# Optimization experiments

Hardware: AMD Instinct MI355X
Metric: run time of the kernel (lower is better)

## Reference

```python
import jax, jax.numpy as jnp
import numpy as np

NB_HEAD = 16
DIM_PER_HEAD = 64
EMB = 1024
B, SQ, SK = 4, 2048, 2048


def setup_inputs() -> dict:
    key = jax.random.key(0)
    ks = jax.random.split(key, 8)
    scale = 1.0 / np.sqrt(EMB)
    return {
        "hidden_state_query": jax.random.normal(ks[0], (B, SQ, EMB), jnp.float32),
        "hidden_state_key": jax.random.normal(ks[1], (B, SK, EMB), jnp.float32),
        "hidden_state_value": jax.random.normal(ks[2], (B, SK, EMB), jnp.float32),
        "attention_mask": jax.random.randint(ks[3], (B, SQ, SK), 0, 2).astype(bool),
        "Wq": jax.random.uniform(ks[4], (NB_HEAD * DIM_PER_HEAD, EMB), jnp.float32, -scale, scale),
        "Wk": jax.random.uniform(ks[5], (NB_HEAD * DIM_PER_HEAD, EMB), jnp.float32, -scale, scale),
        "Wv": jax.random.uniform(ks[6], (NB_HEAD * DIM_PER_HEAD, EMB), jnp.float32, -scale, scale),
        "Wo": jax.random.uniform(ks[7], (EMB, NB_HEAD * DIM_PER_HEAD), jnp.float32, -scale, scale),
    }


def reference(hidden_state_query, hidden_state_key, hidden_state_value,
              attention_mask, Wq, Wk, Wv, Wo):
    bs, sq, _ = hidden_state_query.shape
    sk = hidden_state_key.shape[1]
    # projections (nn.Linear without bias: x @ W.T)
    q = (hidden_state_query @ Wq.T).reshape(bs, sq, NB_HEAD, DIM_PER_HEAD).transpose(0, 2, 1, 3)
    k = (hidden_state_key @ Wk.T).reshape(bs, sk, NB_HEAD, DIM_PER_HEAD).transpose(0, 2, 1, 3)
    v = (hidden_state_value @ Wv.T).reshape(bs, sk, NB_HEAD, DIM_PER_HEAD).transpose(0, 2, 1, 3)
    scores = jnp.einsum('bhqd,bhkd->bhqk', q, k) / jnp.sqrt(jnp.asarray(DIM_PER_HEAD, q.dtype))
    attn = jax.nn.softmax(scores, axis=-1)
    # POST-softmax zero masking (True -> 0), broadcast over heads; no renormalization
    attn = jnp.where(attention_mask[:, None, :, :], jnp.asarray(0.0, attn.dtype), attn)
    ctx = jnp.einsum('bhqk,bhkd->bhqd', attn, v)  # [B,H,Sq,Dh]
    ctx = ctx.transpose(0, 2, 1, 3).reshape(bs, sq, NB_HEAD * DIM_PER_HEAD)
    return ctx @ Wo.T + hidden_state_query
```

## Files before the change

### kernel.cpp

```cpp
#include <hip/hip_runtime.h>
#include <hip/hip_bf16.h>
#include <stdint.h>

typedef __bf16 bf16_t;
typedef bf16_t bf16x2 __attribute__((ext_vector_type(2)));
typedef bf16_t bf16x8 __attribute__((ext_vector_type(8)));
typedef float  f32x4  __attribute__((ext_vector_type(4)));
typedef float  f32x16 __attribute__((ext_vector_type(16)));
typedef unsigned uint2v __attribute__((ext_vector_type(2)));

#define NB_HEAD 16
#define DH      64
#define EMB     1024
#define BATCH   4
#define SEQ     2048
#define NTOK    (BATCH*SEQ)

#define QSCALE 0.1803368801111204f

__device__ __forceinline__ void gload_lds16(const void* g, void* l) {
  __builtin_amdgcn_global_load_lds(
      (const __attribute__((address_space(1))) void*)g,
      (__attribute__((address_space(3))) void*)l, 16, 0, 0);
}

__device__ __forceinline__ uint32_t pkbf(float a, float b) {
  bf16x2 v = { (bf16_t)a, (bf16_t)b };
  return __builtin_bit_cast(uint32_t, v);
}

__device__ __forceinline__ void cvt8_body(const float* __restrict__ in,
                                          bf16_t* __restrict__ out, int i) {
  const float4* p = reinterpret_cast<const float4*>(in) + (size_t)i * 2;
  float4 a = p[0], b = p[1];
  uint4 r;
  r.x = pkbf(a.x, a.y); r.y = pkbf(a.z, a.w);
  r.z = pkbf(b.x, b.y); r.w = pkbf(b.z, b.w);
  reinterpret_cast<uint4*>(out)[i] = r;
}

__device__ __forceinline__ void mkand_body(const uint8_t* __restrict__ m,
                                           uint16_t* __restrict__ out, int i) {
  uint2 v = reinterpret_cast<const uint2*>(m)[i];
  uint4 r;
  uint32_t lo = v.x, hi = v.y;
  uint16_t e[8];
#pragma unroll
  for (int j = 0; j < 4; j++) e[j]     = (uint16_t)(((lo >> (8 * j)) & 0xFF) - 1);
#pragma unroll
  for (int j = 0; j < 4; j++) e[4 + j] = (uint16_t)(((hi >> (8 * j)) & 0xFF) - 1);
  r.x = (uint32_t)e[0] | ((uint32_t)e[1] << 16);
  r.y = (uint32_t)e[2] | ((uint32_t)e[3] << 16);
  r.z = (uint32_t)e[4] | ((uint32_t)e[5] << 16);
  r.w = (uint32_t)e[6] | ((uint32_t)e[7] << 16);
  reinterpret_cast<uint4*>(out)[i] = r;
}

__global__ void __launch_bounds__(256)
prep(const float* __restrict__ Wq, const float* __restrict__ Wk,
     const float* __restrict__ Wv, const float* __restrict__ Wo,
     bf16_t* Wq_b, bf16_t* Wk_b, bf16_t* Wv_b, bf16_t* Wo_b,
     const uint8_t* __restrict__ mask, uint16_t* __restrict__ mand) {
  const int bid = blockIdx.x;
  if (bid < 2048) {
    const int seg = bid >> 9;
    const float* src = seg == 0 ? Wq : seg == 1 ? Wk : seg == 2 ? Wv : Wo;
    bf16_t*      dst = seg == 0 ? Wq_b : seg == 1 ? Wk_b : seg == 2 ? Wv_b : Wo_b;
    cvt8_body(src, dst, (bid & 511) * 256 + (int)threadIdx.x);
  } else {
    mkand_body(mask, mand, (bid - 2048) * 256 + (int)threadIdx.x);
  }
}

#define BM 128
#define BN 128
#define BKT 32

__global__ void __launch_bounds__(256, 2)
gemm_qkv(const float* __restrict__ hq, const float* __restrict__ hk,
         const float* __restrict__ hv,
         const bf16_t* __restrict__ Wq_b, const bf16_t* __restrict__ Wk_b,
         const bf16_t* __restrict__ Wv_b,
         bf16_t* __restrict__ Qb, bf16_t* __restrict__ Kf,
         bf16_t* __restrict__ Vf) {
  __shared__ bf16_t As[2][BM * BKT];
  __shared__ bf16_t Bs[2][BN * BKT];
  const int K = EMB;
  const int z = blockIdx.z;
  const float*  A  = z == 0 ? hq : z == 1 ? hk : hv;
  const bf16_t* Bw = z == 0 ? Wq_b : z == 1 ? Wk_b : Wv_b;

  const int t    = threadIdx.x;
  const int lane = t & 63, w = t >> 6;
  const int wr = w >> 1, wc = w & 1;
  const int l15 = lane & 15, l4 = lane >> 4;

  const int lin = blockIdx.x + 8 * blockIdx.y;
  const int nl  = (lin & 7) * 64 + (lin >> 3);
  const int rowBase = (nl >> 3) * BM, colBase = (nl & 7) * BN;

  f32x4 acc[4][4];
#pragma unroll
  for (int i = 0; i < 4; i++)
#pragma unroll
    for (int j = 0; j < 4; j++) acc[i][j] = f32x4{0.f, 0.f, 0.f, 0.f};

  const int t16 = t * 16;
  const int ar = t >> 1, ac = (t & 1) * 16;
  const float* arow = A + (size_t)(rowBase + ar) * K + ac;
  char* const asdst0 = (char*)As[0] + ar * 64 + ac * 2;
  char* const asdst1 = (char*)As[1] + ar * 64 + ac * 2;

  {
    float4 a0 = *reinterpret_cast<const float4*>(arow);
    float4 a1 = *reinterpret_cast<const float4*>(arow + 4);
    float4 a2 = *reinterpret_cast<const float4*>(arow + 8);
    float4 a3 = *reinterpret_cast<const float4*>(arow + 12);
#pragma unroll
    for (int i = 0; i < 2; ++i) {
      int off = i * 4096 + t16;
      int row = off >> 6, colb = off & 63;
      gload_lds16((const char*)Bw + (((size_t)(colBase + row)) * K) * 2 + colb, (char*)Bs[0] + off);
    }
    uint4 w0, w1;
    w0.x = pkbf(a0.x, a0.y); w0.y = pkbf(a0.z, a0.w);
    w0.z = pkbf(a1.x, a1.y); w0.w = pkbf(a1.z, a1.w);
    w1.x = pkbf(a2.x, a2.y); w1.y = pkbf(a2.z, a2.w);
    w1.z = pkbf(a3.x, a3.y); w1.w = pkbf(a3.z, a3.w);
    *reinterpret_cast<uint4*>(asdst0) = w0;
    *reinterpret_cast<uint4*>(asdst0 + 16) = w1;
  }
  __syncthreads();

  int cur = 0;
  for (int k0 = 0; k0 < K; k0 += BKT) {
    float4 na0, na1, na2, na3;
    const bool more = (k0 + BKT < K);
    if (more) {
      const float* ap = arow + k0 + BKT;
      na0 = *reinterpret_cast<const float4*>(ap);
      na1 = *reinterpret_cast<const float4*>(ap + 4);
      na2 = *reinterpret_cast<const float4*>(ap + 8);
      na3 = *reinterpret_cast<const float4*>(ap + 12);
      const int nb = cur ^ 1;
#pragma unroll
      for (int i = 0; i < 2; ++i) {
        int off = i * 4096 + t16;
        int row = off >> 6, colb = off & 63;
        gload_lds16((const char*)Bw + (((size_t)(colBase + row)) * K + k0 + BKT) * 2 + colb, (char*)Bs[nb] + off);
      }
    }
    {
      bf16x8 af[4], bfb[4];
#pragma unroll
      for (int mi = 0; mi < 4; mi++)
        af[mi] = *reinterpret_cast<const bf16x8*>(
            &As[cur][(wr * 64 + mi * 16 + l15) * BKT + l4 * 8]);
#pragma unroll
      for (int ni = 0; ni < 4; ni++)
        bfb[ni] = *reinterpret_cast<const bf16x8*>(
            &Bs[cur][(wc * 64 + ni * 16 + l15) * BKT + l4 * 8]);
      __builtin_amdgcn_s_setprio(1);
#pragma unroll
      for (int mi = 0; mi < 4; mi++)
#pragma unroll
        for (int ni = 0; ni < 4; ni++)
          acc[mi][ni] = __builtin_amdgcn_mfma_f32_16x16x32_bf16(
              af[mi], bfb[ni], acc[mi][ni], 0, 0, 0);
      __builtin_amdgcn_s_setprio(0);
    }
    if (more) {
      uint4 w0, w1;
      w0.x = pkbf(na0.x, na0.y); w0.y = pkbf(na0.z, na0.w);
      w0.z = pkbf(na1.x, na1.y); w0.w = pkbf(na1.z, na1.w);
      w1.x = pkbf(na2.x, na2.y); w1.y = pkbf(na2.z, na2.w);
      w1.z = pkbf(na3.x, na3.y); w1.w = pkbf(na3.z, na3.w);
      char* d = (cur ? asdst0 : asdst1);
      *reinterpret_cast<uint4*>(d) = w0;
      *reinterpret_cast<uint4*>(d + 16) = w1;
    }
    __syncthreads();
    cur ^= 1;
  }

#pragma unroll
  for (int mi = 0; mi < 4; mi++) {
#pragma unroll
    for (int ni = 0; ni < 4; ni++) {
      const int m0 = rowBase + wr * 64 + mi * 16 + l4 * 4;
      const int n  = colBase + wc * 64 + ni * 16 + l15;
      if (z == 0) {
#pragma unroll
        for (int r = 0; r < 4; r++)
          Qb[(size_t)(m0 + r) * EMB + n] = (bf16_t)(acc[mi][ni][r] * QSCALE);
      } else if (z == 1) {
#pragma unroll
        for (int r = 0; r < 4; r++) {
          int m = m0 + r;
          const int bq = m >> 11, s = m & 2047, hh = n >> 6, d = n & 63;
          size_t local = (size_t)(s >> 6) * 4096 + ((s >> 5) & 1) * 2048 +
                         (d >> 4) * 512 + ((d >> 3) & 1) * 256 + (s & 31) * 8 + (d & 7);
          Kf[(size_t)(bq * 16 + hh) * 131072 + local] = (bf16_t)acc[mi][ni][r];
        }
      } else {
        const int bq = m0 >> 11, s0 = m0 & 2047, hh = n >> 6, d = n & 63;
        size_t local = (size_t)(s0 >> 6) * 4096 + ((s0 >> 4) & 3) * 1024 +
                       (d >> 5) * 512 + ((s0 >> 3) & 1) * 256 + (d & 31) * 8 + (s0 & 7);
        uint2 st;
        st.x = pkbf(acc[mi][ni][0], acc[mi][ni][1]);
        st.y = pkbf(acc[mi][ni][2], acc[mi][ni][3]);
        *reinterpret_cast<uint2*>(Vf + (size_t)(bq * 16 + hh) * 131072 + local) = st;
      }
    }
  }
}

__global__ void __launch_bounds__(256, 4)
gemm_out(const bf16_t* __restrict__ A, const bf16_t* __restrict__ Bw,
         float* __restrict__ Cf, const float* __restrict__ resid) {
  __shared__ bf16_t As[2][BM * BKT];
  __shared__ bf16_t Bs[2][BN * BKT];
  const int K = EMB, N = EMB;
  const int t    = threadIdx.x;
  const int lane = t & 63, w = t >> 6;
  const int wr = w >> 1, wc = w & 1;
  const int l15 = lane & 15, l4 = lane >> 4;

  const int lin = blockIdx.x + 8 * blockIdx.y;
  const int nl  = (lin & 7) * 64 + (lin >> 3);
  const int rowBase = (nl >> 3) * BM, colBase = (nl & 7) * BN;

  f32x4 acc[4][4];
#pragma unroll
  for (int i = 0; i < 4; i++)
#pragma unroll
    for (int j = 0; j < 4; j++) acc[i][j] = f32x4{0.f, 0.f, 0.f, 0.f};

  const int t16 = t * 16;

#pragma unroll
  for (int i = 0; i < 2; ++i) {
    int off = i * 4096 + t16;
    int row = off >> 6, colb = off & 63;
    gload_lds16((const char*)A  + (((size_t)(rowBase + row)) * K) * 2 + colb, (char*)As[0] + off);
    gload_lds16((const char*)Bw + (((size_t)(colBase + row)) * K) * 2 + colb, (char*)Bs[0] + off);
  }
  __syncthreads();

  int cur = 0;
  for (int k0 = 0; k0 < K; k0 += BKT) {
    if (k0 + BKT < K) {
      const int nb = cur ^ 1;
#pragma unroll
      for (int i = 0; i < 2; ++i) {
        int off = i * 4096 + t16;
        int row = off >> 6, colb = off & 63;
        gload_lds16((const char*)A  + (((size_t)(rowBase + row)) * K + k0 + BKT) * 2 + colb, (char*)As[nb] + off);
        gload_lds16((const char*)Bw + (((size_t)(colBase + row)) * K + k0 + BKT) * 2 + colb, (char*)Bs[nb] + off);
      }
    }
    {
      bf16x8 af[4], bfb[4];
#pragma unroll
      for (int mi = 0; mi < 4; mi++)
        af[mi] = *reinterpret_cast<const bf16x8*>(
            &As[cur][(wr * 64 + mi * 16 + l15) * BKT + l4 * 8]);
#pragma unroll
      for (int ni = 0; ni < 4; ni++)
        bfb[ni] = *reinterpret_cast<const bf16x8*>(
            &Bs[cur][(wc * 64 + ni * 16 + l15) * BKT + l4 * 8]);
      __builtin_amdgcn_s_setprio(1);
#pragma unroll
      for (int mi = 0; mi < 4; mi++)
#pragma unroll
        for (int ni = 0; ni < 4; ni++)
          acc[mi][ni] = __builtin_amdgcn_mfma_f32_16x16x32_bf16(
              af[mi], bfb[ni], acc[mi][ni], 0, 0, 0);
      __builtin_amdgcn_s_setprio(0);
    }
    __syncthreads();
    cur ^= 1;
  }

#pragma unroll
  for (int mi = 0; mi < 4; mi++) {
#pragma unroll
    for (int ni = 0; ni < 4; ni++) {
      const int m0 = rowBase + wr * 64 + mi * 16 + l4 * 4;
      const int n  = colBase + wc * 64 + ni * 16 + l15;
#pragma unroll
      for (int r = 0; r < 4; r++) {
        int m = m0 + r;
        Cf[(size_t)m * N + n] = acc[mi][ni][r] + resid[(size_t)m * N + n];
      }
    }
  }
}

__global__ void __launch_bounds__(512, 2)
attn32(const bf16_t* __restrict__ Qb, const bf16_t* __restrict__ Kh,
       const bf16_t* __restrict__ Vt, const uint16_t* __restrict__ Mand,
       bf16_t* __restrict__ ctx) {
  __shared__ __align__(16) bf16_t Ks[2][64 * 64];
  __shared__ __align__(16) bf16_t Vs[2][64 * 64];

  const int t = threadIdx.x, lane = t & 63, wid = t >> 6;
  const int q = lane & 31, hi = lane >> 5;
  const int l16 = lane * 16;

  const int lin = blockIdx.x + 8 * (blockIdx.y + 16 * blockIdx.z);
  const int nl  = (lin & 7) * 64 + (lin >> 3);
  const int bx = nl & 7, h = (nl >> 3) & 15, b = nl >> 7;

  const int q0 = bx * 256 + wid * 32;
  const int qrow = b * SEQ + q0 + q;

  const char* kg = (const char*)(Kh + ((size_t)(b * NB_HEAD + h)) * SEQ * DH);
  const char* vg = (const char*)(Vt + ((size_t)(b * NB_HEAD + h)) * SEQ * DH);

  const bf16_t* qp = Qb + (size_t)qrow * EMB + h * DH + hi * 8;
  bf16x8 qf[4];
#pragma unroll
  for (int d = 0; d < 4; d++) qf[d] = *reinterpret_cast<const bf16x8*>(qp + d * 16);

  f32x16 o0 = {0}, o1 = {0};
  float lrun = 0.f;
  const uint16_t* mbase = Mand + (size_t)qrow * SEQ;

  gload_lds16(kg + t * 16, (char*)Ks[0] + t * 16);
  gload_lds16(vg + t * 16, (char*)Vs[0] + t * 16);
  __syncthreads();

  int cur = 0;
  for (int kb = 0; kb < SEQ; kb += 64) {
    if (kb + 64 < SEQ) {
      const int nb = cur ^ 1;
      gload_lds16(kg + (size_t)(kb + 64) * 128 + t * 16, (char*)Ks[nb] + t * 16);
      gload_lds16(vg + (size_t)(kb + 64) * 128 + t * 16, (char*)Vs[nb] + t * 16);
    }

    const char* kls = (const char*)Ks[cur];
    f32x16 p0 = {0}, p1 = {0};
    __builtin_amdgcn_s_setprio(1);
#pragma unroll
    for (int dsl = 0; dsl < 4; dsl++) {
      bf16x8 kf0 = *reinterpret_cast<const bf16x8*>(kls + dsl * 1024 + l16);
      bf16x8 kf1 = *reinterpret_cast<const bf16x8*>(kls + 4096 + dsl * 1024 + l16);
      p0 = __builtin_amdgcn_mfma_f32_32x32x16_bf16(kf0, qf[dsl], p0, 0, 0, 0);
      p1 = __builtin_amdgcn_mfma_f32_32x32x16_bf16(kf1, qf[dsl], p1, 0, 0, 0);
    }
    __builtin_amdgcn_s_setprio(0);

    uint4 mv[4];
#pragma unroll
    for (int ks = 0; ks < 4; ks++)
      mv[ks] = *reinterpret_cast<const uint4*>(mbase + kb + 16 * ks + 8 * hi);

    float ps = 0.f;
#pragma unroll
    for (int i = 0; i < 16; i++) { p0[i] = __builtin_amdgcn_exp2f(p0[i]); ps += p0[i]; }
#pragma unroll
    for (int i = 0; i < 16; i++) { p1[i] = __builtin_amdgcn_exp2f(p1[i]); ps += p1[i]; }
    ps += __shfl_xor(ps, 32);
    lrun += ps;

    const char* vls = (const char*)Vs[cur];
#pragma unroll
    for (int ks = 0; ks < 4; ks++) {
      const int s8 = (ks & 1) * 8;
      float e0, e1, e2, e3, e4, e5, e6, e7;
      if (ks < 2) {
        e0 = p0[s8+0]; e1 = p0[s8+1]; e2 = p0[s8+2]; e3 = p0[s8+3];
        e4 = p0[s8+4]; e5 = p0[s8+5]; e6 = p0[s8+6]; e7 = p0[s8+7];
      } else {
        e0 = p1[s8+0]; e1 = p1[s8+1]; e2 = p1[s8+2]; e3 = p1[s8+3];
        e4 = p1[s8+4]; e5 = p1[s8+5]; e6 = p1[s8+6]; e7 = p1[s8+7];
      }
      uint32_t a0 = pkbf(e0, e1), a1 = pkbf(e2, e3);
      uint32_t a2 = pkbf(e4, e5), a3 = pkbf(e6, e7);
      uint2v s02 = __builtin_amdgcn_permlane32_swap(a0, a2, false, false);
      uint2v s13 = __builtin_amdgcn_permlane32_swap(a1, a3, false, false);
      uint4 fr;
      fr.x = s02[0]; fr.y = s13[0]; fr.z = s02[1]; fr.w = s13[1];
      fr.x &= mv[ks].x; fr.y &= mv[ks].y; fr.z &= mv[ks].z; fr.w &= mv[ks].w;
      bf16x8 pa = __builtin_bit_cast(bf16x8, fr);
      bf16x8 vf0 = *reinterpret_cast<const bf16x8*>(vls + ks * 2048 + l16);
      bf16x8 vf1 = *reinterpret_cast<const bf16x8*>(vls + ks * 2048 + 1024 + l16);
      __builtin_amdgcn_s_setprio(1);
      o0 = __builtin_amdgcn_mfma_f32_32x32x16_bf16(vf0, pa, o0, 0, 0, 0);
      o1 = __builtin_amdgcn_mfma_f32_32x32x16_bf16(vf1, pa, o1, 0, 0, 0);
      __builtin_amdgcn_s_setprio(0);
    }

    __syncthreads();
    cur ^= 1;
  }

  float inv = 1.0f / lrun;
  bf16_t* cp = ctx + (size_t)qrow * EMB + h * DH;
#pragma unroll
  for (int g = 0; g < 4; g++) {
    uint2 st;
    st.x = pkbf(o0[4*g+0] * inv, o0[4*g+1] * inv);
    st.y = pkbf(o0[4*g+2] * inv, o0[4*g+3] * inv);
    *reinterpret_cast<uint2*>(cp + 8 * g + 4 * hi) = st;
    st.x = pkbf(o1[4*g+0] * inv, o1[4*g+1] * inv);
    st.y = pkbf(o1[4*g+2] * inv, o1[4*g+3] * inv);
    *reinterpret_cast<uint2*>(cp + 32 + 8 * g + 4 * hi) = st;
  }
}

extern "C" void kernel_launch(void* const* d_in, const int* in_sizes, int n_in,
                              void* d_out, int out_size, void* d_ws, size_t ws_size,
                              hipStream_t stream) {
  const float*   hq   = (const float*)d_in[0];
  const float*   hk   = (const float*)d_in[1];
  const float*   hv   = (const float*)d_in[2];
  const uint8_t* mask = (const uint8_t*)d_in[3];
  const float*   Wq   = (const float*)d_in[4];
  const float*   Wk   = (const float*)d_in[5];
  const float*   Wv   = (const float*)d_in[6];
  const float*   Wo   = (const float*)d_in[7];
  float* out = (float*)d_out;

  char* ws = (char*)d_ws;
  const size_t MI = 1024 * 1024;
  uint16_t* Mand = (uint16_t*)(ws);
  bf16_t* Qb   = (bf16_t*)(ws + 32 * MI);
  bf16_t* Kf   = (bf16_t*)(ws + 48 * MI);
  bf16_t* Vf   = (bf16_t*)(ws + 64 * MI);
  bf16_t* ctx  = (bf16_t*)(ws + 80 * MI);
  bf16_t* Wq_b = (bf16_t*)(ws + 96 * MI);
  bf16_t* Wk_b = (bf16_t*)(ws + 98 * MI);
  bf16_t* Wv_b = (bf16_t*)(ws + 100 * MI);
  bf16_t* Wo_b = (bf16_t*)(ws + 102 * MI);

  prep<<<10240, 256, 0, stream>>>(Wq, Wk, Wv, Wo,
                                  Wq_b, Wk_b, Wv_b, Wo_b, mask, Mand);

  gemm_qkv<<<dim3(8, 64, 3), 256, 0, stream>>>(hq, hk, hv,
                                               Wq_b, Wk_b, Wv_b, Qb, Kf, Vf);

  attn32<<<dim3(SEQ / 256, NB_HEAD, BATCH), 512, 0, stream>>>(Qb, Kf, Vf, Mand, ctx);

  gemm_out<<<dim3(8, 64), 256, 0, stream>>>(ctx, Wo_b, out, hq);
}
```

Baseline: 245.6 us.

## Pre-convert hidden states to bf16 in prep and use async LDS loads in QKV GEMM

The prep kernel now also converts the three fp32 hidden-state inputs to bf16 in workspace. The QKV GEMM can then load both operands with direct global-to-LDS copies instead of fp32 register loads plus in-loop packing, and its occupancy hint rises to 4. The workspace layout is rebuilt, and the mask expansion moves to a separate kernel when the workspace is too small. This adds an extra read and write pass over the activations, trading that traffic for a simpler, more asynchronous GEMM inner loop.

```diff
diff --git a/kernel.cpp b/kernel.cpp
--- a/kernel.cpp
+++ b/kernel.cpp
@@ -57,37 +57,51 @@
 }
 
 __global__ void __launch_bounds__(256)
-prep(const float* __restrict__ Wq, const float* __restrict__ Wk,
-     const float* __restrict__ Wv, const float* __restrict__ Wo,
+prep(const float* __restrict__ hq, const float* __restrict__ hk,
+     const float* __restrict__ hv, const float* __restrict__ Wq,
+     const float* __restrict__ Wk, const float* __restrict__ Wv,
+     const float* __restrict__ Wo,
+     bf16_t* hq_b, bf16_t* hk_b, bf16_t* hv_b,
      bf16_t* Wq_b, bf16_t* Wk_b, bf16_t* Wv_b, bf16_t* Wo_b,
      const uint8_t* __restrict__ mask, uint16_t* __restrict__ mand) {
   const int bid = blockIdx.x;
-  if (bid < 2048) {
-    const int seg = bid >> 9;
+  if (bid < 12288) {
+    const int seg = bid >> 12;
+    const float* src = seg == 0 ? hq : seg == 1 ? hk : hv;
+    bf16_t*      dst = seg == 0 ? hq_b : seg == 1 ? hk_b : hv_b;
+    cvt8_body(src, dst, (bid & 4095) * 256 + (int)threadIdx.x);
+  } else if (bid < 14336) {
+    const int sb = bid - 12288;
+    const int seg = sb >> 9;
     const float* src = seg == 0 ? Wq : seg == 1 ? Wk : seg == 2 ? Wv : Wo;
     bf16_t*      dst = seg == 0 ? Wq_b : seg == 1 ? Wk_b : seg == 2 ? Wv_b : Wo_b;
-    cvt8_body(src, dst, (bid & 511) * 256 + (int)threadIdx.x);
+    cvt8_body(src, dst, (sb & 511) * 256 + (int)threadIdx.x);
   } else {
-    mkand_body(mask, mand, (bid - 2048) * 256 + (int)threadIdx.x);
-  }
+    mkand_body(mask, mand, (bid - 14336) * 256 + (int)threadIdx.x);
+  }
+}
+
+__global__ void __launch_bounds__(256)
+mkand(const uint8_t* __restrict__ m, uint16_t* __restrict__ out) {
+  mkand_body(m, out, blockIdx.x * 256 + (int)threadIdx.x);
 }
 
 #define BM 128
 #define BN 128
 #define BKT 32
 
-__global__ void __launch_bounds__(256, 2)
-gemm_qkv(const float* __restrict__ hq, const float* __restrict__ hk,
-         const float* __restrict__ hv,
-         const bf16_t* __restrict__ Wq_b, const bf16_t* __restrict__ Wk_b,
-         const bf16_t* __restrict__ Wv_b,
-         bf16_t* __restrict__ Qb, bf16_t* __restrict__ Kf,
-         bf16_t* __restrict__ Vf) {
+__global__ void __launch_bounds__(256, 4)
+gemm_qkv3(const bf16_t* __restrict__ hq_b, const bf16_t* __restrict__ hk_b,
+          const bf16_t* __restrict__ hv_b,
+          const bf16_t* __restrict__ Wq_b, const bf16_t* __restrict__ Wk_b,
+          const bf16_t* __restrict__ Wv_b,
+          bf16_t* __restrict__ Qb, bf16_t* __restrict__ Kf,
+          bf16_t* __restrict__ Vf) {
   __shared__ bf16_t As[2][BM * BKT];
   __shared__ bf16_t Bs[2][BN * BKT];
-  const int K = EMB;
+  const int K = EMB, N = EMB;
   const int z = blockIdx.z;
-  const float*  A  = z == 0 ? hq : z == 1 ? hk : hv;
+  const bf16_t* A  = z == 0 ? hq_b : z == 1 ? hk_b : hv_b;
   const bf16_t* Bw = z == 0 ? Wq_b : z == 1 ? Wk_b : Wv_b;
 
   const int t    = threadIdx.x;
@@ -106,47 +120,25 @@
     for (int j = 0; j < 4; j++) acc[i][j] = f32x4{0.f, 0.f, 0.f, 0.f};
 
   const int t16 = t * 16;
-  const int ar = t >> 1, ac = (t & 1) * 16;
-  const float* arow = A + (size_t)(rowBase + ar) * K + ac;
-  char* const asdst0 = (char*)As[0] + ar * 64 + ac * 2;
-  char* const asdst1 = (char*)As[1] + ar * 64 + ac * 2;
-
-  {
-    float4 a0 = *reinterpret_cast<const float4*>(arow);
-    float4 a1 = *reinterpret_cast<const float4*>(arow + 4);
-    float4 a2 = *reinterpret_cast<const float4*>(arow + 8);
-    float4 a3 = *reinterpret_cast<const float4*>(arow + 12);
-#pragma unroll
-    for (int i = 0; i < 2; ++i) {
-      int off = i * 4096 + t16;
-      int row = off >> 6, colb = off & 63;
-      gload_lds16((const char*)Bw + (((size_t)(colBase + row)) * K) * 2 + colb, (char*)Bs[0] + off);
-    }
-    uint4 w0, w1;
-    w0.x = pkbf(a0.x, a0.y); w0.y = pkbf(a0.z, a0.w);
-    w0.z = pkbf(a1.x, a1.y); w0.w = pkbf(a1.z, a1.w);
-    w1.x = pkbf(a2.x, a2.y); w1.y = pkbf(a2.z, a2.w);
-    w1.z = pkbf(a3.x, a3.y); w1.w = pkbf(a3.z, a3.w);
-    *reinterpret_cast<uint4*>(asdst0) = w0;
-    *reinterpret_cast<uint4*>(asdst0 + 16) = w1;
+
+#pragma unroll
+  for (int i = 0; i < 2; ++i) {
+    int off  = i * 4096 + t16;
+    int row  = off >> 6, colb = off & 63;
+    gload_lds16((const char*)A  + (((size_t)(rowBase + row)) * K) * 2 + colb, (char*)As[0] + off);
+    gload_lds16((const char*)Bw + (((size_t)(colBase + row)) * K) * 2 + colb, (char*)Bs[0] + off);
   }
   __syncthreads();
 
   int cur = 0;
   for (int k0 = 0; k0 < K; k0 += BKT) {
-    float4 na0, na1, na2, na3;
-    const bool more = (k0 + BKT < K);
-    if (more) {
-      const float* ap = arow + k0 + BKT;
-      na0 = *reinterpret_cast<const float4*>(ap);
-      na1 = *reinterpret_cast<const float4*>(ap + 4);
-      na2 = *reinterpret_cast<const float4*>(ap + 8);
-      na3 = *reinterpret_cast<const float4*>(ap + 12);
+    if (k0 + BKT < K) {
       const int nb = cur ^ 1;
 #pragma unroll
       for (int i = 0; i < 2; ++i) {
-        int off = i * 4096 + t16;
-        int row = off >> 6, colb = off & 63;
+        int off  = i * 4096 + t16;
+        int row  = off >> 6, colb = off & 63;
+        gload_lds16((const char*)A  + (((size_t)(rowBase + row)) * K + k0 + BKT) * 2 + colb, (char*)As[nb] + off);
         gload_lds16((const char*)Bw + (((size_t)(colBase + row)) * K + k0 + BKT) * 2 + colb, (char*)Bs[nb] + off);
       }
     }
@@ -168,16 +160,6 @@
           acc[mi][ni] = __builtin_amdgcn_mfma_f32_16x16x32_bf16(
               af[mi], bfb[ni], acc[mi][ni], 0, 0, 0);
       __builtin_amdgcn_s_setprio(0);
-    }
-    if (more) {
-      uint4 w0, w1;
-      w0.x = pkbf(na0.x, na0.y); w0.y = pkbf(na0.z, na0.w);
-      w0.z = pkbf(na1.x, na1.y); w0.w = pkbf(na1.z, na1.w);
-      w1.x = pkbf(na2.x, na2.y); w1.y = pkbf(na2.z, na2.w);
-      w1.z = pkbf(na3.x, na3.y); w1.w = pkbf(na3.z, na3.w);
-      char* d = (cur ? asdst0 : asdst1);
-      *reinterpret_cast<uint4*>(d) = w0;
-      *reinterpret_cast<uint4*>(d + 16) = w1;
     }
     __syncthreads();
     cur ^= 1;
@@ -240,8 +222,8 @@
 
 #pragma unroll
   for (int i = 0; i < 2; ++i) {
-    int off = i * 4096 + t16;
-    int row = off >> 6, colb = off & 63;
+    int off  = i * 4096 + t16;
+    int row  = off >> 6, colb = off & 63;
     gload_lds16((const char*)A  + (((size_t)(rowBase + row)) * K) * 2 + colb, (char*)As[0] + off);
     gload_lds16((const char*)Bw + (((size_t)(colBase + row)) * K) * 2 + colb, (char*)Bs[0] + off);
   }
@@ -253,8 +235,8 @@
       const int nb = cur ^ 1;
 #pragma unroll
       for (int i = 0; i < 2; ++i) {
-        int off = i * 4096 + t16;
-        int row = off >> 6, colb = off & 63;
+        int off  = i * 4096 + t16;
+        int row  = off >> 6, colb = off & 63;
         gload_lds16((const char*)A  + (((size_t)(rowBase + row)) * K + k0 + BKT) * 2 + colb, (char*)As[nb] + off);
         gload_lds16((const char*)Bw + (((size_t)(colBase + row)) * K + k0 + BKT) * 2 + colb, (char*)Bs[nb] + off);
       }
@@ -424,22 +406,33 @@
   float* out = (float*)d_out;
 
   char* ws = (char*)d_ws;
-  const size_t MI = 1024 * 1024;
-  uint16_t* Mand = (uint16_t*)(ws);
-  bf16_t* Qb   = (bf16_t*)(ws + 32 * MI);
-  bf16_t* Kf   = (bf16_t*)(ws + 48 * MI);
-  bf16_t* Vf   = (bf16_t*)(ws + 64 * MI);
-  bf16_t* ctx  = (bf16_t*)(ws + 80 * MI);
-  bf16_t* Wq_b = (bf16_t*)(ws + 96 * MI);
-  bf16_t* Wk_b = (bf16_t*)(ws + 98 * MI);
-  bf16_t* Wv_b = (bf16_t*)(ws + 100 * MI);
-  bf16_t* Wo_b = (bf16_t*)(ws + 102 * MI);
-
-  prep<<<10240, 256, 0, stream>>>(Wq, Wk, Wv, Wo,
-                                  Wq_b, Wk_b, Wv_b, Wo_b, mask, Mand);
-
-  gemm_qkv<<<dim3(8, 64, 3), 256, 0, stream>>>(hq, hk, hv,
-                                               Wq_b, Wk_b, Wv_b, Qb, Kf, Vf);
+  const size_t SZ_H = (size_t)NTOK * EMB * 2;
+  const size_t SZ_W = (size_t)EMB * EMB * 2;
+  bf16_t* hq_b = (bf16_t*)(ws + 0 * SZ_H);
+  bf16_t* hk_b = (bf16_t*)(ws + 1 * SZ_H);
+  bf16_t* hv_b = (bf16_t*)(ws + 2 * SZ_H);
+  bf16_t* Qb   = (bf16_t*)(ws + 3 * SZ_H);
+  bf16_t* Kf   = (bf16_t*)(ws + 4 * SZ_H);
+  bf16_t* Vf   = (bf16_t*)(ws + 5 * SZ_H);
+  bf16_t* ctx  = (bf16_t*)(ws + 6 * SZ_H);
+  bf16_t* Wq_b = (bf16_t*)(ws + 7 * SZ_H + 0 * SZ_W);
+  bf16_t* Wk_b = (bf16_t*)(ws + 7 * SZ_H + 1 * SZ_W);
+  bf16_t* Wv_b = (bf16_t*)(ws + 7 * SZ_H + 2 * SZ_W);
+  bf16_t* Wo_b = (bf16_t*)(ws + 7 * SZ_H + 3 * SZ_W);
+
+  const size_t MAND_OFF = 7 * SZ_H + 4 * SZ_W;
+  const size_t MAND_SZ  = (size_t)BATCH * SEQ * SEQ * 2;
+  const bool bigws = ws_size >= MAND_OFF + MAND_SZ;
+  uint16_t* Mand = bigws ? (uint16_t*)(ws + MAND_OFF) : (uint16_t*)ws;
+
+  prep<<<bigws ? 22528 : 14336, 256, 0, stream>>>(
+      hq, hk, hv, Wq, Wk, Wv, Wo,
+      hq_b, hk_b, hv_b, Wq_b, Wk_b, Wv_b, Wo_b, mask, Mand);
+
+  gemm_qkv3<<<dim3(8, 64, 3), 256, 0, stream>>>(hq_b, hk_b, hv_b,
+                                                Wq_b, Wk_b, Wv_b, Qb, Kf, Vf);
+
+  if (!bigws) mkand<<<8192, 256, 0, stream>>>(mask, Mand);
 
   attn32<<<dim3(SEQ / 256, NB_HEAD, BATCH), 512, 0, stream>>>(Qb, Kf, Vf, Mand, ctx);
 
```

Measured after the change: 229.7 us. -6.5%, faster.
